# Kernel tuning notes

Measured on AMD Instinct MI355X. Metric: run time of the kernel, lower is better.

The kernel has to match this reference:

```python
import jax, jax.numpy as jnp
import numpy as np

BETA = 0.25

def setup_inputs() -> dict:
    key = jax.random.key(0)
    k1, k2 = jax.random.split(key)
    N, K, D = 262144, 256, 256
    z_e = jax.random.normal(k1, (N, D), dtype=jnp.float32)
    # nn.Embedding init: uniform(-1/K, 1/K)
    emb_weight = jax.random.uniform(k2, (K, D), dtype=jnp.float32, minval=-1.0 / K, maxval=1.0 / K)
    return {"z_e": z_e, "emb_weight": emb_weight}

def reference(z_e, emb_weight):
    # squared L2 distances: ||z||^2 + ||e||^2 - 2 z e^T  -> [N, K]
    dist = (jnp.sum(z_e ** 2, axis=1, keepdims=True)
            + jnp.sum(emb_weight ** 2, axis=1)
            - 2.0 * jnp.matmul(z_e, emb_weight.T))
    encoding_inds = jnp.argmin(dist, axis=1)  # [N]
    z_q = emb_weight[encoding_inds]           # [N, D]

    sg = jax.lax.stop_gradient
    commitment_loss = jnp.mean((sg(z_e) - z_q) ** 2)
    codebook_loss = jnp.mean((z_e - sg(z_q)) ** 2)
    loss = codebook_loss + BETA * commitment_loss

    # straight-through estimator
    z_q_st = z_e + sg(z_q - z_e)
    return z_q_st, encoding_inds, loss
```

## Files before the change

### kernel.cpp

```cpp
#include <hip/hip_runtime.h>

typedef __attribute__((ext_vector_type(8))) short bf16x8;
typedef __attribute__((ext_vector_type(4))) float f32x4;
typedef __attribute__((ext_vector_type(4))) unsigned short us4;
typedef __attribute__((ext_vector_type(8))) unsigned short us8;

#define NROWS 262144
#define KC 256
#define DD 256
#define BM 64
#define DK 32
#define SW 40
#define TAU 1.5e-3f
#define FCAP 65536

__device__ __forceinline__ float np_pw128_sq(const float* a) {
    float r[8];
#pragma unroll
    for (int j = 0; j < 8; ++j) r[j] = __fmul_rn(a[j], a[j]);
    for (int i = 8; i < 128; i += 8) {
#pragma unroll
        for (int j = 0; j < 8; ++j)
            r[j] = __fadd_rn(r[j], __fmul_rn(a[i + j], a[i + j]));
    }
    float t01 = __fadd_rn(r[0], r[1]), t23 = __fadd_rn(r[2], r[3]);
    float t45 = __fadd_rn(r[4], r[5]), t67 = __fadd_rn(r[6], r[7]);
    return __fadd_rn(__fadd_rn(t01, t23), __fadd_rn(t45, t67));
}
__device__ __forceinline__ float np_sum256_sq(const float* a) {
    return __fadd_rn(np_pw128_sq(a), np_pw128_sq(a + 128));
}

__device__ __forceinline__ unsigned short bf16_rne(float x) {
    unsigned b = __float_as_uint(x);
    b += 0x7FFFu + ((b >> 16) & 1u);
    return (unsigned short)(b >> 16);
}

__global__ void vq_prep(const float* __restrict__ emb, float* __restrict__ se,
                        double* __restrict__ accum, int* __restrict__ gcnt) {
    int k = threadIdx.x;
    if (k == 0) { *accum = 0.0; *gcnt = 0; }
    se[k] = np_sum256_sq(emb + (size_t)k * DD);
}

__global__ void vq_split(const float* __restrict__ emb, unsigned short* __restrict__ ph) {
    int f = (blockIdx.x * 256 + threadIdx.x) * 4;
    float4 v = *reinterpret_cast<const float4*>(emb + f);
    int k = f >> 8, d = f & 255;
    int off = (d >> 5) * (KC * DK) + k * DK + (d & 31);
    us4 h;
    h[0] = bf16_rne(v.x); h[1] = bf16_rne(v.y);
    h[2] = bf16_rne(v.z); h[3] = bf16_rne(v.w);
    *reinterpret_cast<us4*>(ph + off) = h;
}

__global__ __launch_bounds__(256, 4)
void vq_main(const float* __restrict__ ze, const float* __restrict__ emb,
             const unsigned short* __restrict__ ph,
             const float* __restrict__ se_g, float* __restrict__ out_zq,
             float* __restrict__ out_inds, double* __restrict__ accum,
             int* __restrict__ glist, int* __restrict__ gcnt)
{
    __shared__ __attribute__((aligned(16))) unsigned short zs_hi[BM * SW];
    __shared__ __attribute__((aligned(16))) unsigned short es_hi[KC * SW];
    __shared__ float  se_s[KC];
    __shared__ int    inds_s[BM];

    float* wv1 = reinterpret_cast<float*>(es_hi);
    float* wv2 = wv1 + 4 * BM;
    int*   wk1 = reinterpret_cast<int*>(wv2 + 4 * BM);
    float* red = reinterpret_cast<float*>(zs_hi);

    const int t = threadIdx.x;
    const int w = t >> 6;
    const int l = t & 63;
    const int q = (t >> 4) & 3;
    const int c = t & 15;
    const size_t m0 = (size_t)blockIdx.x * BM;
    const float* zbase = ze + m0 * DD;

    se_s[t] = se_g[t];

    f32x4 acc[4][4];
#pragma unroll
    for (int i = 0; i < 4; ++i)
#pragma unroll
        for (int j = 0; j < 4; ++j) acc[i][j] = (f32x4){0.f, 0.f, 0.f, 0.f};
    float sz_acc = 0.f;

    const int r0 = t >> 3, c40 = t & 7;
    const int r1 = (256 + t) >> 3, c41 = t & 7;

    float4 zva = *reinterpret_cast<const float4*>(zbase + (size_t)r0 * DD + c40 * 4);
    float4 zvb = *reinterpret_cast<const float4*>(zbase + (size_t)r1 * DD + c41 * 4);

    for (int dci = 0; dci < 8; ++dci) {
        const int dc = dci * DK;
        __syncthreads();
        const unsigned short* ehp = ph + dci * (KC * DK);
#pragma unroll
        for (int it = 0; it < 4; ++it) {
            int idx = it * 256 + t;
            int row = idx >> 2, c8 = idx & 3;
            us8 h = *reinterpret_cast<const us8*>(ehp + idx * 8);
            *reinterpret_cast<us8*>(&es_hi[row * SW + c8 * 8]) = h;
        }
        {
            sz_acc = fmaf(zva.x, zva.x, sz_acc); sz_acc = fmaf(zva.y, zva.y, sz_acc);
            sz_acc = fmaf(zva.z, zva.z, sz_acc); sz_acc = fmaf(zva.w, zva.w, sz_acc);
            us4 h;
            h[0] = bf16_rne(zva.x); h[1] = bf16_rne(zva.y);
            h[2] = bf16_rne(zva.z); h[3] = bf16_rne(zva.w);
            *reinterpret_cast<us4*>(&zs_hi[r0 * SW + c40 * 4]) = h;
        }
        {
            sz_acc = fmaf(zvb.x, zvb.x, sz_acc); sz_acc = fmaf(zvb.y, zvb.y, sz_acc);
            sz_acc = fmaf(zvb.z, zvb.z, sz_acc); sz_acc = fmaf(zvb.w, zvb.w, sz_acc);
            us4 h;
            h[0] = bf16_rne(zvb.x); h[1] = bf16_rne(zvb.y);
            h[2] = bf16_rne(zvb.z); h[3] = bf16_rne(zvb.w);
            *reinterpret_cast<us4*>(&zs_hi[r1 * SW + c41 * 4]) = h;
        }
        if (dci < 7) {
            zva = *reinterpret_cast<const float4*>(zbase + (size_t)r0 * DD + dc + DK + c40 * 4);
            zvb = *reinterpret_cast<const float4*>(zbase + (size_t)r1 * DD + dc + DK + c41 * 4);
        }
        __syncthreads();
        bf16x8 a_hi[4], b_hi[4];
#pragma unroll
        for (int mf = 0; mf < 4; ++mf)
            a_hi[mf] = *reinterpret_cast<const bf16x8*>(&zs_hi[(16 * mf + c) * SW + q * 8]);
#pragma unroll
        for (int nf = 0; nf < 4; ++nf)
            b_hi[nf] = *reinterpret_cast<const bf16x8*>(&es_hi[(64 * w + 16 * nf + c) * SW + q * 8]);
#pragma unroll
        for (int mf = 0; mf < 4; ++mf)
#pragma unroll
            for (int nf = 0; nf < 4; ++nf)
                acc[mf][nf] = __builtin_amdgcn_mfma_f32_16x16x32_bf16(a_hi[mf], b_hi[nf], acc[mf][nf], 0, 0, 0);
    }
    __syncthreads();

#pragma unroll
    for (int mf = 0; mf < 4; ++mf)
#pragma unroll
        for (int j = 0; j < 4; ++j) {
            float v1 = 3.4e38f, v2 = 3.4e38f; int k1 = 0x7fffffff;
#pragma unroll
            for (int nf = 0; nf < 4; ++nf) {
                int k = 64 * w + 16 * nf + c;
                float dv = fmaf(-2.f, acc[mf][nf][j], se_s[k]);
                if (dv < v1) { v2 = v1; v1 = dv; k1 = k; }
                else if (dv < v2) { v2 = dv; }
            }
#pragma unroll
            for (int off = 1; off < 16; off <<= 1) {
                float ov1 = __shfl_xor(v1, off, 64);
                float ov2 = __shfl_xor(v2, off, 64);
                int   ok1 = __shfl_xor(k1, off, 64);
                bool other = (ov1 < v1) || (ov1 == v1 && ok1 < k1);
                float nv2 = other ? fminf(v1, ov2) : fminf(v2, ov1);
                if (other) { v1 = ov1; k1 = ok1; }
                v2 = nv2;
            }
            if (c == 0) {
                int row = 16 * mf + 4 * q + j;
                wv1[w * BM + row] = v1; wv2[w * BM + row] = v2; wk1[w * BM + row] = k1;
            }
        }
    __syncthreads();

    float lossv = 0.f;
    if (t < BM) {
        float v1 = wv1[t], v2 = wv2[t]; int k1 = wk1[t];
#pragma unroll
        for (int ww = 1; ww < 4; ++ww) {
            float ov1 = wv1[ww * BM + t], ov2 = wv2[ww * BM + t];
            int ok1 = wk1[ww * BM + t];
            bool other = (ov1 < v1) || (ov1 == v1 && ok1 < k1);
            float nv2 = other ? fminf(v1, ov2) : fminf(v2, ov1);
            if (other) { v1 = ov1; k1 = ok1; }
            v2 = nv2;
        }
        inds_s[t] = k1;
        lossv = v1;
        if (v2 - v1 < TAU) {
            int s = atomicAdd(gcnt, 1);
            if (s < FCAP) glist[s] = (int)(m0 + t);
        }
    }
    __syncthreads();

    if (t < BM) out_inds[m0 + t] = (float)inds_s[t];

    for (int r = w; r < BM; r += 4) {
        int k = inds_s[r];
        float4 v = *reinterpret_cast<const float4*>(emb + (size_t)k * DD + l * 4);
        *reinterpret_cast<float4*>(out_zq + (m0 + r) * DD + l * 4) = v;
    }

    red[t] = sz_acc + lossv;
    __syncthreads();
    for (int s = 128; s > 0; s >>= 1) {
        if (t < s) red[t] += red[t + s];
        __syncthreads();
    }
    if (t == 0) atomicAdd(accum, (double)red[0]);
}

__global__ __launch_bounds__(256)
void vq_fix(const float* __restrict__ ze, const float* __restrict__ emb,
            const float* __restrict__ se_g, const int* __restrict__ glist,
            const int* __restrict__ gcnt, float* __restrict__ out_zq,
            float* __restrict__ out_inds)
{
    __shared__ float dq[16][256];
    __shared__ float srow_s[16];
    __shared__ int   rowid_s[16];
    __shared__ int   klds[16];

    const int t = threadIdx.x;
    int F = *gcnt; if (F > FCAP) F = FCAP;
    const float se_k = se_g[t];
    const float4* e4p = reinterpret_cast<const float4*>(emb + (size_t)t * DD);

    for (int g = blockIdx.x * 16; g < F; g += gridDim.x * 16) {
        __syncthreads();
        if (t < 16) {
            int idx = g + t; if (idx > F - 1) idx = F - 1;
            int row = glist[idx];
            rowid_s[t] = row;
            srow_s[t] = np_sum256_sq(ze + (size_t)row * DD);
        }
        __syncthreads();

        const float* zp[16];
#pragma unroll
        for (int r = 0; r < 16; ++r)
            zp[r] = ze + (size_t)__builtin_amdgcn_readfirstlane(rowid_s[r]) * DD;

        float m32[16];
#pragma unroll
        for (int r = 0; r < 16; ++r) m32[r] = 0.f;
        for (int d4 = 0; d4 < 64; ++d4) {
            float4 e4 = e4p[d4];
            const int d = d4 * 4;
#pragma unroll
            for (int r = 0; r < 16; ++r) {
                m32[r] = __fmaf_rn(zp[r][d + 0], e4.x, m32[r]);
                m32[r] = __fmaf_rn(zp[r][d + 1], e4.y, m32[r]);
                m32[r] = __fmaf_rn(zp[r][d + 2], e4.z, m32[r]);
                m32[r] = __fmaf_rn(zp[r][d + 3], e4.w, m32[r]);
            }
        }
#pragma unroll
        for (int r = 0; r < 16; ++r) {
            float A = __fadd_rn(srow_s[r], se_k);
            dq[r][t] = __fsub_rn(A, __fmul_rn(2.0f, m32[r]));
        }
        __syncthreads();

        {
            const int r = t >> 4, p = t & 15;
            float bv = 3.4e38f; int bk = 0x7fffffff;
#pragma unroll
            for (int i = 0; i < 16; ++i) {
                int k = p * 16 + i;
                float v = dq[r][k];
                if (v < bv) { bv = v; bk = k; }
            }
#pragma unroll
            for (int off = 1; off < 16; off <<= 1) {
                float ov = __shfl_xor(bv, off, 64);
                int   ok = __shfl_xor(bk, off, 64);
                if (ov < bv || (ov == bv && ok < bk)) { bv = ov; bk = ok; }
            }
            if (p == 0) klds[r] = bk;
        }
        __syncthreads();

        int R = F - g; if (R > 16) R = 16;
#pragma unroll
        for (int r = 0; r < 16; ++r) {
            if (r < R) {
                int row = rowid_s[r];
                int kk  = klds[r];
                out_zq[(size_t)row * DD + t] = emb[(size_t)kk * DD + t];
                if (t == 0) out_inds[row] = (float)kk;
            }
        }
    }
}

__global__ void vq_fin(const double* __restrict__ accum, float* __restrict__ out_loss) {
    *out_loss = (float)(1.25 * (*accum) / ((double)NROWS * (double)DD));
}

extern "C" void kernel_launch(void* const* d_in, const int* in_sizes, int n_in,
                              void* d_out, int out_size, void* d_ws, size_t ws_size,
                              hipStream_t stream) {
    const float* ze  = (const float*)d_in[0];
    const float* emb = (const float*)d_in[1];
    float* out      = (float*)d_out;
    float* out_zq   = out;
    float* out_inds = out + (size_t)NROWS * DD;
    float* out_loss = out + (size_t)NROWS * DD + NROWS;

    double* accum = (double*)d_ws;
    int*    gcnt  = (int*)((char*)d_ws + 8);
    float*  se    = (float*)((char*)d_ws + 256);
    int*    glist = (int*)((char*)d_ws + 4096);
    unsigned short* ph = (unsigned short*)((char*)d_ws + 4096 + 262144);

    vq_prep<<<1, 256, 0, stream>>>(emb, se, accum, gcnt);
    vq_split<<<KC * DD / (256 * 4), 256, 0, stream>>>(emb, ph);
    vq_main<<<NROWS / BM, 256, 0, stream>>>(ze, emb, ph, se, out_zq, out_inds,
                                            accum, glist, gcnt);
    vq_fix<<<1024, 256, 0, stream>>>(ze, emb, se, glist, gcnt, out_zq, out_inds);
    vq_fin<<<1, 1, 0, stream>>>(accum, out_loss);
}
```

Before: 332.3 us.

## Repartition MFMA work so each wave owns 16 rows across all codewords

Each wave now computes a 16-row by 256-codeword tile instead of 64 rows by 64 codewords. The A fragments are loaded straight from global into registers and converted to bf16 there, which removes the z shared-memory staging and the cross-wave argmin merge. Codebook chunks are prefetched into registers one step ahead to overlap global loads with the MFMAs. The trade-off is much higher register pressure (64 accumulator floats plus all 8 A fragments and 16 float4 z loads), with the occupancy hint of 4 blocks removed. Each wave also reads 16 B fragments from LDS per step rather than 4.

After: 367.7 us. +10.7%, slower.

```diff
diff --git a/kernel.cpp b/kernel.cpp
--- a/kernel.cpp
+++ b/kernel.cpp
@@ -55,22 +55,17 @@
     *reinterpret_cast<us4*>(ph + off) = h;
 }
 
-__global__ __launch_bounds__(256, 4)
+__global__ __launch_bounds__(256)
 void vq_main(const float* __restrict__ ze, const float* __restrict__ emb,
              const unsigned short* __restrict__ ph,
              const float* __restrict__ se_g, float* __restrict__ out_zq,
              float* __restrict__ out_inds, double* __restrict__ accum,
              int* __restrict__ glist, int* __restrict__ gcnt)
 {
-    __shared__ __attribute__((aligned(16))) unsigned short zs_hi[BM * SW];
     __shared__ __attribute__((aligned(16))) unsigned short es_hi[KC * SW];
     __shared__ float  se_s[KC];
     __shared__ int    inds_s[BM];
-
-    float* wv1 = reinterpret_cast<float*>(es_hi);
-    float* wv2 = wv1 + 4 * BM;
-    int*   wk1 = reinterpret_cast<int*>(wv2 + 4 * BM);
-    float* red = reinterpret_cast<float*>(zs_hi);
+    __shared__ float  red[256];
 
     const int t = threadIdx.x;
     const int w = t >> 6;
@@ -78,126 +73,112 @@
     const int q = (t >> 4) & 3;
     const int c = t & 15;
     const size_t m0 = (size_t)blockIdx.x * BM;
-    const float* zbase = ze + m0 * DD;
 
     se_s[t] = se_g[t];
 
-    f32x4 acc[4][4];
-#pragma unroll
-    for (int i = 0; i < 4; ++i)
-#pragma unroll
-        for (int j = 0; j < 4; ++j) acc[i][j] = (f32x4){0.f, 0.f, 0.f, 0.f};
+    const unsigned short* ehp0 = ph;
+    us8 ereg[4];
+#pragma unroll
+    for (int it = 0; it < 4; ++it)
+        ereg[it] = *reinterpret_cast<const us8*>(ehp0 + (it * 256 + t) * 8);
+
+    const float* zrow = ze + (m0 + 16 * w + c) * DD + q * 8;
+    float4 zlo[8], zhi[8];
+#pragma unroll
+    for (int dci = 0; dci < 8; ++dci) {
+        zlo[dci] = *reinterpret_cast<const float4*>(zrow + dci * 32);
+        zhi[dci] = *reinterpret_cast<const float4*>(zrow + dci * 32 + 4);
+    }
+
     float sz_acc = 0.f;
-
-    const int r0 = t >> 3, c40 = t & 7;
-    const int r1 = (256 + t) >> 3, c41 = t & 7;
-
-    float4 zva = *reinterpret_cast<const float4*>(zbase + (size_t)r0 * DD + c40 * 4);
-    float4 zvb = *reinterpret_cast<const float4*>(zbase + (size_t)r1 * DD + c41 * 4);
-
+    bf16x8 afrag[8];
+#pragma unroll
     for (int dci = 0; dci < 8; ++dci) {
-        const int dc = dci * DK;
-        __syncthreads();
-        const unsigned short* ehp = ph + dci * (KC * DK);
-#pragma unroll
-        for (int it = 0; it < 4; ++it) {
-            int idx = it * 256 + t;
-            int row = idx >> 2, c8 = idx & 3;
-            us8 h = *reinterpret_cast<const us8*>(ehp + idx * 8);
-            *reinterpret_cast<us8*>(&es_hi[row * SW + c8 * 8]) = h;
-        }
-        {
-            sz_acc = fmaf(zva.x, zva.x, sz_acc); sz_acc = fmaf(zva.y, zva.y, sz_acc);
-            sz_acc = fmaf(zva.z, zva.z, sz_acc); sz_acc = fmaf(zva.w, zva.w, sz_acc);
-            us4 h;
-            h[0] = bf16_rne(zva.x); h[1] = bf16_rne(zva.y);
-            h[2] = bf16_rne(zva.z); h[3] = bf16_rne(zva.w);
-            *reinterpret_cast<us4*>(&zs_hi[r0 * SW + c40 * 4]) = h;
-        }
-        {
-            sz_acc = fmaf(zvb.x, zvb.x, sz_acc); sz_acc = fmaf(zvb.y, zvb.y, sz_acc);
-            sz_acc = fmaf(zvb.z, zvb.z, sz_acc); sz_acc = fmaf(zvb.w, zvb.w, sz_acc);
-            us4 h;
-            h[0] = bf16_rne(zvb.x); h[1] = bf16_rne(zvb.y);
-            h[2] = bf16_rne(zvb.z); h[3] = bf16_rne(zvb.w);
-            *reinterpret_cast<us4*>(&zs_hi[r1 * SW + c41 * 4]) = h;
-        }
+        float4 a = zlo[dci], b = zhi[dci];
+        sz_acc = fmaf(a.x, a.x, sz_acc); sz_acc = fmaf(a.y, a.y, sz_acc);
+        sz_acc = fmaf(a.z, a.z, sz_acc); sz_acc = fmaf(a.w, a.w, sz_acc);
+        sz_acc = fmaf(b.x, b.x, sz_acc); sz_acc = fmaf(b.y, b.y, sz_acc);
+        sz_acc = fmaf(b.z, b.z, sz_acc); sz_acc = fmaf(b.w, b.w, sz_acc);
+        us8 h;
+        h[0] = bf16_rne(a.x); h[1] = bf16_rne(a.y); h[2] = bf16_rne(a.z); h[3] = bf16_rne(a.w);
+        h[4] = bf16_rne(b.x); h[5] = bf16_rne(b.y); h[6] = bf16_rne(b.z); h[7] = bf16_rne(b.w);
+        afrag[dci] = __builtin_bit_cast(bf16x8, h);
+    }
+
+#pragma unroll
+    for (int it = 0; it < 4; ++it) {
+        int idx = it * 256 + t;
+        *reinterpret_cast<us8*>(&es_hi[(idx >> 2) * SW + (idx & 3) * 8]) = ereg[it];
+    }
+
+    f32x4 acc[16];
+#pragma unroll
+    for (int i = 0; i < 16; ++i) acc[i] = (f32x4){0.f, 0.f, 0.f, 0.f};
+
+#pragma unroll
+    for (int dci = 0; dci < 8; ++dci) {
+        __syncthreads();
         if (dci < 7) {
-            zva = *reinterpret_cast<const float4*>(zbase + (size_t)r0 * DD + dc + DK + c40 * 4);
-            zvb = *reinterpret_cast<const float4*>(zbase + (size_t)r1 * DD + dc + DK + c41 * 4);
-        }
-        __syncthreads();
-        bf16x8 a_hi[4], b_hi[4];
-#pragma unroll
-        for (int mf = 0; mf < 4; ++mf)
-            a_hi[mf] = *reinterpret_cast<const bf16x8*>(&zs_hi[(16 * mf + c) * SW + q * 8]);
-#pragma unroll
-        for (int nf = 0; nf < 4; ++nf)
-            b_hi[nf] = *reinterpret_cast<const bf16x8*>(&es_hi[(64 * w + 16 * nf + c) * SW + q * 8]);
-#pragma unroll
-        for (int mf = 0; mf < 4; ++mf)
-#pragma unroll
-            for (int nf = 0; nf < 4; ++nf)
-                acc[mf][nf] = __builtin_amdgcn_mfma_f32_16x16x32_bf16(a_hi[mf], b_hi[nf], acc[mf][nf], 0, 0, 0);
-    }
-    __syncthreads();
-
-#pragma unroll
-    for (int mf = 0; mf < 4; ++mf)
-#pragma unroll
-        for (int j = 0; j < 4; ++j) {
-            float v1 = 3.4e38f, v2 = 3.4e38f; int k1 = 0x7fffffff;
-#pragma unroll
-            for (int nf = 0; nf < 4; ++nf) {
-                int k = 64 * w + 16 * nf + c;
-                float dv = fmaf(-2.f, acc[mf][nf][j], se_s[k]);
-                if (dv < v1) { v2 = v1; v1 = dv; k1 = k; }
-                else if (dv < v2) { v2 = dv; }
-            }
-#pragma unroll
-            for (int off = 1; off < 16; off <<= 1) {
-                float ov1 = __shfl_xor(v1, off, 64);
-                float ov2 = __shfl_xor(v2, off, 64);
-                int   ok1 = __shfl_xor(k1, off, 64);
-                bool other = (ov1 < v1) || (ov1 == v1 && ok1 < k1);
-                float nv2 = other ? fminf(v1, ov2) : fminf(v2, ov1);
-                if (other) { v1 = ov1; k1 = ok1; }
-                v2 = nv2;
-            }
-            if (c == 0) {
-                int row = 16 * mf + 4 * q + j;
-                wv1[w * BM + row] = v1; wv2[w * BM + row] = v2; wk1[w * BM + row] = k1;
-            }
-        }
-    __syncthreads();
+            const unsigned short* ehp = ph + (dci + 1) * (KC * DK);
+#pragma unroll
+            for (int it = 0; it < 4; ++it)
+                ereg[it] = *reinterpret_cast<const us8*>(ehp + (it * 256 + t) * 8);
+        }
+#pragma unroll
+        for (int nf = 0; nf < 16; ++nf) {
+            bf16x8 b = *reinterpret_cast<const bf16x8*>(&es_hi[(16 * nf + c) * SW + q * 8]);
+            acc[nf] = __builtin_amdgcn_mfma_f32_16x16x32_bf16(afrag[dci], b, acc[nf], 0, 0, 0);
+        }
+        __syncthreads();
+        if (dci < 7) {
+#pragma unroll
+            for (int it = 0; it < 4; ++it) {
+                int idx = it * 256 + t;
+                *reinterpret_cast<us8*>(&es_hi[(idx >> 2) * SW + (idx & 3) * 8]) = ereg[it];
+            }
+        }
+    }
 
     float lossv = 0.f;
-    if (t < BM) {
-        float v1 = wv1[t], v2 = wv2[t]; int k1 = wk1[t];
-#pragma unroll
-        for (int ww = 1; ww < 4; ++ww) {
-            float ov1 = wv1[ww * BM + t], ov2 = wv2[ww * BM + t];
-            int ok1 = wk1[ww * BM + t];
+#pragma unroll
+    for (int j = 0; j < 4; ++j) {
+        float v1 = 3.4e38f, v2 = 3.4e38f; int k1 = 0x7fffffff;
+#pragma unroll
+        for (int nf = 0; nf < 16; ++nf) {
+            int k = 16 * nf + c;
+            float dv = fmaf(-2.f, acc[nf][j], se_s[k]);
+            if (dv < v1) { v2 = v1; v1 = dv; k1 = k; }
+            else if (dv < v2) { v2 = dv; }
+        }
+#pragma unroll
+        for (int off = 1; off < 16; off <<= 1) {
+            float ov1 = __shfl_xor(v1, off, 64);
+            float ov2 = __shfl_xor(v2, off, 64);
+            int   ok1 = __shfl_xor(k1, off, 64);
             bool other = (ov1 < v1) || (ov1 == v1 && ok1 < k1);
             float nv2 = other ? fminf(v1, ov2) : fminf(v2, ov1);
             if (other) { v1 = ov1; k1 = ok1; }
             v2 = nv2;
         }
-        inds_s[t] = k1;
-        lossv = v1;
-        if (v2 - v1 < TAU) {
-            int s = atomicAdd(gcnt, 1);
-            if (s < FCAP) glist[s] = (int)(m0 + t);
+        if (c == 0) {
+            int row = 16 * w + 4 * q + j;
+            inds_s[row] = k1;
+            lossv += v1;
+            if (v2 - v1 < TAU) {
+                int s = atomicAdd(gcnt, 1);
+                if (s < FCAP) glist[s] = (int)(m0 + row);
+            }
         }
     }
     __syncthreads();
 
     if (t < BM) out_inds[m0 + t] = (float)inds_s[t];
 
-    for (int r = w; r < BM; r += 4) {
-        int k = inds_s[r];
+#pragma unroll
+    for (int r = 0; r < 16; ++r) {
+        int k = inds_s[16 * w + r];
         float4 v = *reinterpret_cast<const float4*>(emb + (size_t)k * DD + l * 4);
-        *reinterpret_cast<float4*>(out_zq + (m0 + r) * DD + l * 4) = v;
+        *reinterpret_cast<float4*>(out_zq + (m0 + 16 * w + r) * DD + l * 4) = v;
     }
 
     red[t] = sz_acc + lossv;
```
